# Kernel tuning notes

Measured on AMD Instinct MI355X. Metric: run time of the kernel, lower is better.

## Reference

```python
import jax, jax.numpy as jnp
import numpy as np

NUM_ITERATIONS = 3
EPS = 1e-7


def squash(t, axis=-1):
    # scale = |t|^2/(1+|t|^2), unit = t/sqrt(|t|^2+eps)
    sn = jnp.sum(t * t, axis=axis, keepdims=True)
    return (sn / (1.0 + sn)) * t / jnp.sqrt(sn + EPS)


def setup_inputs() -> dict:
    key = jax.random.key(0)
    kx, kw = jax.random.split(key)
    B, R, CIN = 256, 1152, 8
    C, COUT = 10, 16
    x = jax.random.normal(kx, (B, R, CIN), dtype=jnp.float32)
    W = jax.random.normal(kw, (C, R, CIN, COUT), dtype=jnp.float32)
    return {"x": x, "W": W}


def reference(x, W):
    # u_hat = x[None,:,:,None,:] @ W[:,None]  -> [C, B, R, 1, O]
    u_hat = jnp.einsum('bri,crio->cbro', x, W)[:, :, :, None, :]
    b = jnp.zeros_like(u_hat)  # logits over route nodes, full u_hat shape (faithful)
    outputs = None
    for i in range(NUM_ITERATIONS):
        c = jax.nn.softmax(b, axis=2)  # softmax over route nodes R
        outputs = squash(jnp.sum(c * u_hat, axis=2, keepdims=True))  # [C,B,1,1,O]
        if i != NUM_ITERATIONS - 1:
            # agreement: dot over out channels, broadcast back onto b
            b = b + jnp.sum(u_hat * outputs, axis=-1, keepdims=True)
    return outputs
```

## Files before the change

kernel.cpp:

```cpp
#include <hip/hip_runtime.h>
#include <hip/hip_fp16.h>

#define RDIM 1152
#define CIN  8
#define COUT 16
#define CDIM 10
#define BDIM 256
#define EPS 1e-7f

#define ARB 64
#define ABB 16
#define NRBLK (RDIM / ARB)
#define NBBLK (BDIM / ABB)
#define ANWG (CDIM * NRBLK * NBBLK)
#define XSTRIDE 12

__global__ __launch_bounds__(256) void caps_uhat(
    const float* __restrict__ x, const float* __restrict__ W,
    __half* __restrict__ uh)
{
    const int orig = blockIdx.x;
    const int id   = (orig & 7) * (ANWG / 8) + (orig >> 3);
    const int c    = id % CDIM;
    const int chnk = id / CDIM;
    const int rblk = chnk >> 4;
    const int bblk = chnk & 15;
    const int r0   = rblk * ARB;
    const int b0   = bblk * ABB;

    const int t    = threadIdx.x;
    const int half = t >> 7;
    const int u    = t & 127;
    const int rl   = u >> 1;
    const int oh   = u & 1;

    __shared__ float xs[ABB * ARB * XSTRIDE];

    {
        const float* xsrc = x + ((size_t)b0 * RDIM + r0) * CIN;
        #pragma unroll
        for (int k = 0; k < 8; ++k) {
            const int uu = t + k * 256;
            const int bl = uu >> 7;
            const int q  = uu & 127;
            float4 v = *(const float4*)(xsrc + (size_t)bl * RDIM * CIN + q * 4);
            *(float4*)&xs[(bl * ARB + (q >> 1)) * XSTRIDE + (q & 1) * 4] = v;
        }
    }

    float w0[8], w1[8], w2[8], w3[8], w4[8], w5[8], w6[8], w7[8];
    {
        const float* wb = W + ((size_t)c * RDIM + r0 + rl) * (CIN * COUT) + oh * 8;
        #define LDW(I, DST)                                                   \
        {                                                                     \
            float4 lo = *(const float4*)(wb + (I) * COUT);                    \
            float4 hi = *(const float4*)(wb + (I) * COUT + 4);                \
            DST[0] = lo.x; DST[1] = lo.y; DST[2] = lo.z; DST[3] = lo.w;       \
            DST[4] = hi.x; DST[5] = hi.y; DST[6] = hi.z; DST[7] = hi.w;       \
        }
        LDW(0, w0) LDW(1, w1) LDW(2, w2) LDW(3, w3)
        LDW(4, w4) LDW(5, w5) LDW(6, w6) LDW(7, w7)
        #undef LDW
    }
    asm volatile("" :
        "+v"(w0[0]), "+v"(w0[1]), "+v"(w0[2]), "+v"(w0[3]),
        "+v"(w0[4]), "+v"(w0[5]), "+v"(w0[6]), "+v"(w0[7]),
        "+v"(w1[0]), "+v"(w1[1]), "+v"(w1[2]), "+v"(w1[3]),
        "+v"(w1[4]), "+v"(w1[5]), "+v"(w1[6]), "+v"(w1[7]));
    asm volatile("" :
        "+v"(w2[0]), "+v"(w2[1]), "+v"(w2[2]), "+v"(w2[3]),
        "+v"(w2[4]), "+v"(w2[5]), "+v"(w2[6]), "+v"(w2[7]),
        "+v"(w3[0]), "+v"(w3[1]), "+v"(w3[2]), "+v"(w3[3]),
        "+v"(w3[4]), "+v"(w3[5]), "+v"(w3[6]), "+v"(w3[7]));
    asm volatile("" :
        "+v"(w4[0]), "+v"(w4[1]), "+v"(w4[2]), "+v"(w4[3]),
        "+v"(w4[4]), "+v"(w4[5]), "+v"(w4[6]), "+v"(w4[7]),
        "+v"(w5[0]), "+v"(w5[1]), "+v"(w5[2]), "+v"(w5[3]),
        "+v"(w5[4]), "+v"(w5[5]), "+v"(w5[6]), "+v"(w5[7]));
    asm volatile("" :
        "+v"(w6[0]), "+v"(w6[1]), "+v"(w6[2]), "+v"(w6[3]),
        "+v"(w6[4]), "+v"(w6[5]), "+v"(w6[6]), "+v"(w6[7]),
        "+v"(w7[0]), "+v"(w7[1]), "+v"(w7[2]), "+v"(w7[3]),
        "+v"(w7[4]), "+v"(w7[5]), "+v"(w7[6]), "+v"(w7[7]));

    __syncthreads();

    __half* ubase = uh + (((size_t)c * BDIM + b0 + half * 8) * RDIM + r0 + rl) * COUT
                  + oh * 8;
    const size_t ustep = (size_t)RDIM * COUT;
    const float* xrow = &xs[(half * 8 * ARB + rl) * XSTRIDE];

    #pragma unroll
    for (int bl = 0; bl < ABB / 2; ++bl) {
        const float* xp = xrow + bl * (ARB * XSTRIDE);
        float4 p0 = *(const float4*)(xp);
        float4 p1 = *(const float4*)(xp + 4);

        float a0 = p0.x * w0[0];
        float a1 = p0.x * w0[1];
        float a2 = p0.x * w0[2];
        float a3 = p0.x * w0[3];
        float a4 = p0.x * w0[4];
        float a5 = p0.x * w0[5];
        float a6 = p0.x * w0[6];
        float a7 = p0.x * w0[7];
        #define FMA8(XI, WR)                                                  \
            a0 = fmaf((XI), WR[0], a0); a1 = fmaf((XI), WR[1], a1);           \
            a2 = fmaf((XI), WR[2], a2); a3 = fmaf((XI), WR[3], a3);           \
            a4 = fmaf((XI), WR[4], a4); a5 = fmaf((XI), WR[5], a5);           \
            a6 = fmaf((XI), WR[6], a6); a7 = fmaf((XI), WR[7], a7);
        FMA8(p0.y, w1) FMA8(p0.z, w2) FMA8(p0.w, w3)
        FMA8(p1.x, w4) FMA8(p1.y, w5) FMA8(p1.z, w6) FMA8(p1.w, w7)
        #undef FMA8

        __half2 h0 = __floats2half2_rn(a0, a1), h1 = __floats2half2_rn(a2, a3);
        __half2 h2 = __floats2half2_rn(a4, a5), h3 = __floats2half2_rn(a6, a7);
        uint4 packed = make_uint4(*(const unsigned*)&h0, *(const unsigned*)&h1,
                                  *(const unsigned*)&h2, *(const unsigned*)&h3);
        *(uint4*)(ubase + bl * ustep) = packed;
    }
}

#define BUNIT 18

__global__ __launch_bounds__(256) void caps_route2(
    const __half* __restrict__ uh, float* __restrict__ out)
{
    const int cb   = blockIdx.x;
    const int t    = threadIdx.x;
    const int lane = t & 63;
    const int wave = t >> 6;
    const int oq   = t & 3;
    const int rsub = t >> 2;

    __shared__ uint2 uhs[RDIM * COUT / 4];
    __shared__ float red[4][20];
    __shared__ __align__(16) float vout[COUT];

    const uint4* src = (const uint4*)(uh + (size_t)cb * RDIM * COUT);
    uint4* dst = (uint4*)uhs;
    float sp[8] = {0.f, 0.f, 0.f, 0.f, 0.f, 0.f, 0.f, 0.f};
    #pragma unroll
    for (int k = 0; k < 9; ++k) {
        uint4 v = src[t + k * 256];
        dst[t + k * 256] = v;
        float2 f0 = __half22float2(*(const __half2*)&v.x);
        float2 f1 = __half22float2(*(const __half2*)&v.y);
        float2 f2 = __half22float2(*(const __half2*)&v.z);
        float2 f3 = __half22float2(*(const __half2*)&v.w);
        sp[0] += f0.x; sp[1] += f0.y; sp[2] += f1.x; sp[3] += f1.y;
        sp[4] += f2.x; sp[5] += f2.y; sp[6] += f3.x; sp[7] += f3.y;
    }
    #pragma unroll
    for (int off = 2; off <= 32; off <<= 1) {
        #pragma unroll
        for (int j = 0; j < 8; ++j) sp[j] += __shfl_xor(sp[j], off);
    }
    if (lane < 2) {
        #pragma unroll
        for (int j = 0; j < 8; ++j) red[wave][lane * 8 + j] = sp[j];
    }
    __syncthreads();

    if (wave == 0 && lane < COUT) {
        float s = 0.f;
        #pragma unroll
        for (int w2 = 0; w2 < 4; ++w2) s += red[w2][lane];
        s *= (1.0f / (float)RDIM);
        float sn = s * s;
        #pragma unroll
        for (int off = 1; off < 16; off <<= 1) sn += __shfl_xor(sn, off);
        const float scale = (sn / (1.0f + sn)) / sqrtf(sn + EPS);
        vout[lane] = s * scale;
    }
    __syncthreads();

    float bb[BUNIT];
    #pragma unroll
    for (int k = 0; k < BUNIT; ++k) bb[k] = 0.f;

    #pragma unroll
    for (int it = 1; it <= 2; ++it) {
        const float4 vq = *(const float4*)&vout[oq * 4];
        float Zp = 0.f, s0 = 0.f, s1 = 0.f, s2 = 0.f, s3 = 0.f;
        #pragma unroll
        for (int k = 0; k < BUNIT; ++k) {
            const int r = k * 64 + rsub;
            uint2 raw = uhs[r * 4 + oq];
            float2 fA = __half22float2(*(const __half2*)&raw.x);
            float2 fB = __half22float2(*(const __half2*)&raw.y);
            float a = fA.x * vq.x;
            a = fmaf(fA.y, vq.y, a);
            a = fmaf(fB.x, vq.z, a);
            a = fmaf(fB.y, vq.w, a);
            a += __shfl_xor(a, 1);
            a += __shfl_xor(a, 2);
            bb[k] += a;
            float e = __expf(bb[k]);
            Zp += e;
            s0 = fmaf(e, fA.x, s0); s1 = fmaf(e, fA.y, s1);
            s2 = fmaf(e, fB.x, s2); s3 = fmaf(e, fB.y, s3);
        }
        #pragma unroll
        for (int off = 32; off >= 4; off >>= 1) {
            Zp += __shfl_xor(Zp, off);
            s0 += __shfl_xor(s0, off);
            s1 += __shfl_xor(s1, off);
            s2 += __shfl_xor(s2, off);
            s3 += __shfl_xor(s3, off);
        }
        if (lane < 4) {
            red[wave][lane * 4 + 0] = s0;
            red[wave][lane * 4 + 1] = s1;
            red[wave][lane * 4 + 2] = s2;
            red[wave][lane * 4 + 3] = s3;
            if (lane == 0) red[wave][16] = Zp;
        }
        __syncthreads();
        if (wave == 0 && lane < COUT) {
            float Z = 0.f;
            #pragma unroll
            for (int w2 = 0; w2 < 4; ++w2) Z += red[w2][16];
            float s = 0.f;
            #pragma unroll
            for (int w2 = 0; w2 < 4; ++w2) s += red[w2][lane];
            s /= Z;
            float sn = s * s;
            #pragma unroll
            for (int off = 1; off < 16; off <<= 1) sn += __shfl_xor(sn, off);
            const float scale = (sn / (1.0f + sn)) / sqrtf(sn + EPS);
            vout[lane] = s * scale;
        }
        __syncthreads();
    }

    if (t < 4) {
        float* op = out + (size_t)cb * COUT + t * 4;
        *(float4*)op = *(const float4*)&vout[t * 4];
    }
}

#define NB   2
#define FBLOCK 384
#define FUNITS 12
#define FNW (FBLOCK / 64)
#define NPAIR (BDIM / NB)
#define FNWG (CDIM * NPAIR)

__global__ __launch_bounds__(FBLOCK) void caps_route_fused(
    const float* __restrict__ x, const float* __restrict__ W,
    float* __restrict__ out)
{
    const int orig = blockIdx.x;
    const int wg   = (orig & 7) * (FNWG / 8) + (orig >> 3);
    const int c    = wg / NPAIR;
    const int b0   = (wg % NPAIR) * NB;
    const int tid  = threadIdx.x;
    const int lane = tid & 63;
    const int wave = tid >> 6;
    const int oq   = tid & 3;
    const int rsub = tid >> 2;

    __shared__ uint2 uhT[NB][4][1156];
    __shared__ float red[NB][FNW][COUT];
    __shared__ float scalz[NB][FNW];
    __shared__ __align__(16) float vout[NB][COUT];

    const float* __restrict__ Wc  = W + (size_t)c * RDIM * CIN * COUT;
    const float* __restrict__ xb0 = x + (size_t)b0 * RDIM * CIN;
    const float* __restrict__ xb1 = xb0 + RDIM * CIN;

    #pragma unroll
    for (int k = 0; k < FUNITS; ++k) {
        const int r = k * 96 + rsub;
        const float4* xq0 = (const float4*)(xb0 + (size_t)r * CIN);
        const float4* xq1 = (const float4*)(xb1 + (size_t)r * CIN);
        float4 p00 = xq0[0], p01 = xq0[1];
        float4 p10 = xq1[0], p11 = xq1[1];
        float xr0[CIN] = {p00.x, p00.y, p00.z, p00.w, p01.x, p01.y, p01.z, p01.w};
        float xr1[CIN] = {p10.x, p10.y, p10.z, p10.w, p11.x, p11.y, p11.z, p11.w};
        const float* wrow = Wc + (size_t)r * (CIN * COUT) + oq * 4;
        float a00 = 0.f, a01 = 0.f, a02 = 0.f, a03 = 0.f;
        float a10 = 0.f, a11 = 0.f, a12 = 0.f, a13 = 0.f;
        #pragma unroll
        for (int i = 0; i < CIN; ++i) {
            float4 w = *(const float4*)(wrow + i * COUT);
            a00 = fmaf(xr0[i], w.x, a00); a01 = fmaf(xr0[i], w.y, a01);
            a02 = fmaf(xr0[i], w.z, a02); a03 = fmaf(xr0[i], w.w, a03);
            a10 = fmaf(xr1[i], w.x, a10); a11 = fmaf(xr1[i], w.y, a11);
            a12 = fmaf(xr1[i], w.z, a12); a13 = fmaf(xr1[i], w.w, a13);
        }
        __half2 hA0 = __floats2half2_rn(a00, a01), hB0 = __floats2half2_rn(a02, a03);
        __half2 hA1 = __floats2half2_rn(a10, a11), hB1 = __floats2half2_rn(a12, a13);
        uhT[0][oq][r] = make_uint2(*(const unsigned*)&hA0, *(const unsigned*)&hB0);
        uhT[1][oq][r] = make_uint2(*(const unsigned*)&hA1, *(const unsigned*)&hB1);
    }
    __syncthreads();

    float bb0[FUNITS], bb1[FUNITS];
    #pragma unroll
    for (int k = 0; k < FUNITS; ++k) { bb0[k] = 0.f; bb1[k] = 0.f; }

    #pragma unroll
    for (int it = 0; it < 3; ++it) {
        float Zp0 = 0.f, s00 = 0.f, s01 = 0.f, s02 = 0.f, s03 = 0.f;
        float Zp1 = 0.f, s10 = 0.f, s11 = 0.f, s12 = 0.f, s13 = 0.f;
        #pragma unroll
        for (int k = 0; k < FUNITS; ++k) {
            const int r = k * 96 + rsub;
            float e0 = __expf(bb0[k]);
            float e1 = __expf(bb1[k]);
            uint2 r0 = uhT[0][oq][r], r1 = uhT[1][oq][r];
            float2 fA0 = __half22float2(*(const __half2*)&r0.x);
            float2 fB0 = __half22float2(*(const __half2*)&r0.y);
            float2 fA1 = __half22float2(*(const __half2*)&r1.x);
            float2 fB1 = __half22float2(*(const __half2*)&r1.y);
            Zp0 += e0; Zp1 += e1;
            s00 = fmaf(e0, fA0.x, s00); s01 = fmaf(e0, fA0.y, s01);
            s02 = fmaf(e0, fB0.x, s02); s03 = fmaf(e0, fB0.y, s03);
            s10 = fmaf(e1, fA1.x, s10); s11 = fmaf(e1, fA1.y, s11);
            s12 = fmaf(e1, fB1.x, s12); s13 = fmaf(e1, fB1.y, s13);
        }
        #pragma unroll
        for (int off = 32; off >= 4; off >>= 1) {
            Zp0 += __shfl_xor(Zp0, off);  Zp1 += __shfl_xor(Zp1, off);
            s00 += __shfl_xor(s00, off);  s10 += __shfl_xor(s10, off);
            s01 += __shfl_xor(s01, off);  s11 += __shfl_xor(s11, off);
            s02 += __shfl_xor(s02, off);  s12 += __shfl_xor(s12, off);
            s03 += __shfl_xor(s03, off);  s13 += __shfl_xor(s13, off);
        }
        if (lane < 4) {
            red[0][wave][lane * 4 + 0] = s00; red[0][wave][lane * 4 + 1] = s01;
            red[0][wave][lane * 4 + 2] = s02; red[0][wave][lane * 4 + 3] = s03;
            red[1][wave][lane * 4 + 0] = s10; red[1][wave][lane * 4 + 1] = s11;
            red[1][wave][lane * 4 + 2] = s12; red[1][wave][lane * 4 + 3] = s13;
            if (lane == 0) { scalz[0][wave] = Zp0; scalz[1][wave] = Zp1; }
        }
        __syncthreads();
        if (wave == 0 && (lane & 31) < COUT) {
            const int nb = lane >> 5;
            const int o  = lane & 15;
            float Z = 0.f;
            #pragma unroll
            for (int w2 = 0; w2 < FNW; ++w2) Z += scalz[nb][w2];
            float s = 0.f;
            #pragma unroll
            for (int w2 = 0; w2 < FNW; ++w2) s += red[nb][w2][o];
            s /= Z;
            float sn = s * s;
            #pragma unroll
            for (int off = 1; off < 16; off <<= 1) sn += __shfl_xor(sn, off);
            const float scale = (sn / (1.0f + sn)) / sqrtf(sn + EPS);
            vout[nb][o] = s * scale;
        }
        __syncthreads();
        if (it < 2) {
            const float4 v0 = *(const float4*)&vout[0][oq * 4];
            const float4 v1 = *(const float4*)&vout[1][oq * 4];
            #pragma unroll
            for (int k = 0; k < FUNITS; ++k) {
                const int r = k * 96 + rsub;
                uint2 r0 = uhT[0][oq][r], r1 = uhT[1][oq][r];
                float2 fA0 = __half22float2(*(const __half2*)&r0.x);
                float2 fB0 = __half22float2(*(const __half2*)&r0.y);
                float2 fA1 = __half22float2(*(const __half2*)&r1.x);
                float2 fB1 = __half22float2(*(const __half2*)&r1.y);
                float a0 = fA0.x * v0.x;
                a0 = fmaf(fA0.y, v0.y, a0);
                a0 = fmaf(fB0.x, v0.z, a0);
                a0 = fmaf(fB0.y, v0.w, a0);
                float a1 = fA1.x * v1.x;
                a1 = fmaf(fA1.y, v1.y, a1);
                a1 = fmaf(fB1.x, v1.z, a1);
                a1 = fmaf(fB1.y, v1.w, a1);
                a0 += __shfl_xor(a0, 1);  a1 += __shfl_xor(a1, 1);
                a0 += __shfl_xor(a0, 2);  a1 += __shfl_xor(a1, 2);
                bb0[k] += a0;
                bb1[k] += a1;
            }
        }
    }
    if (tid < 8) {
        const int nb = tid >> 2, q = tid & 3;
        float* op = out + ((size_t)c * BDIM + b0 + nb) * COUT + q * 4;
        *(float4*)op = *(const float4*)&vout[nb][q * 4];
    }
}

extern "C" void kernel_launch(void* const* d_in, const int* in_sizes, int n_in,
                              void* d_out, int out_size, void* d_ws, size_t ws_size,
                              hipStream_t stream) {
    const float* x = (const float*)d_in[0];
    const float* W = (const float*)d_in[1];
    float* out = (float*)d_out;

    const size_t UH_BYTES = (size_t)CDIM * BDIM * RDIM * COUT * sizeof(__half);
    if (ws_size >= UH_BYTES) {
        __half* uh = (__half*)d_ws;
        caps_uhat<<<ANWG, 256, 0, stream>>>(x, W, uh);
        caps_route2<<<CDIM * BDIM, 256, 0, stream>>>(uh, out);
    } else {
        caps_route_fused<<<FNWG, FBLOCK, 0, stream>>>(x, W, out);
    }
}
```

Before: 56.14 us.

## Retile u_hat kernel to reuse x tile across five capsule classes

The u_hat kernel now tiles 16 route nodes by 32 batch rows and loops over five output classes per workgroup, loading the x tile into shared memory once and reusing it for each class. Before, every class had its own workgroup that reloaded x. This cuts redundant x traffic and reduces the grid to 1152 workgroups, each doing more serial work. The trade is that W loads are now serialized inside a non-unrolled loop, with less parallelism available to hide their latency.

```diff
diff --git a/kernel.cpp b/kernel.cpp
--- a/kernel.cpp
+++ b/kernel.cpp
@@ -8,11 +8,12 @@
 #define BDIM 256
 #define EPS 1e-7f
 
-#define ARB 64
-#define ABB 16
+#define ARB 16
+#define ABB 32
 #define NRBLK (RDIM / ARB)
 #define NBBLK (BDIM / ABB)
-#define ANWG (CDIM * NRBLK * NBBLK)
+#define NCG   2
+#define ANWG (NRBLK * NBBLK * NCG)
 #define XSTRIDE 12
 
 __global__ __launch_bounds__(256) void caps_uhat(
@@ -21,103 +22,110 @@
 {
     const int orig = blockIdx.x;
     const int id   = (orig & 7) * (ANWG / 8) + (orig >> 3);
-    const int c    = id % CDIM;
-    const int chnk = id / CDIM;
-    const int rblk = chnk >> 4;
-    const int bblk = chnk & 15;
+    const int cg   = id & 1;
+    const int rem  = id >> 1;
+    const int bblk = rem & 7;
+    const int rblk = rem >> 3;
     const int r0   = rblk * ARB;
     const int b0   = bblk * ABB;
 
-    const int t    = threadIdx.x;
-    const int half = t >> 7;
-    const int u    = t & 127;
-    const int rl   = u >> 1;
-    const int oh   = u & 1;
+    const int t  = threadIdx.x;
+    const int u  = t & 31;
+    const int rl = u >> 1;
+    const int oh = u & 1;
+    const int bg = t >> 5;
 
     __shared__ float xs[ABB * ARB * XSTRIDE];
 
     {
-        const float* xsrc = x + ((size_t)b0 * RDIM + r0) * CIN;
-        #pragma unroll
-        for (int k = 0; k < 8; ++k) {
-            const int uu = t + k * 256;
-            const int bl = uu >> 7;
-            const int q  = uu & 127;
-            float4 v = *(const float4*)(xsrc + (size_t)bl * RDIM * CIN + q * 4);
+        #pragma unroll
+        for (int k = 0; k < 4; ++k) {
+            const int unit = t + k * 256;
+            const int bl   = unit >> 5;
+            const int q    = unit & 31;
+            float4 v = *(const float4*)(
+                x + ((size_t)(b0 + bl) * RDIM + r0) * CIN + q * 4);
             *(float4*)&xs[(bl * ARB + (q >> 1)) * XSTRIDE + (q & 1) * 4] = v;
         }
     }
-
-    float w0[8], w1[8], w2[8], w3[8], w4[8], w5[8], w6[8], w7[8];
-    {
-        const float* wb = W + ((size_t)c * RDIM + r0 + rl) * (CIN * COUT) + oh * 8;
-        #define LDW(I, DST)                                                   \
-        {                                                                     \
-            float4 lo = *(const float4*)(wb + (I) * COUT);                    \
-            float4 hi = *(const float4*)(wb + (I) * COUT + 4);                \
-            DST[0] = lo.x; DST[1] = lo.y; DST[2] = lo.z; DST[3] = lo.w;       \
-            DST[4] = hi.x; DST[5] = hi.y; DST[6] = hi.z; DST[7] = hi.w;       \
-        }
-        LDW(0, w0) LDW(1, w1) LDW(2, w2) LDW(3, w3)
-        LDW(4, w4) LDW(5, w5) LDW(6, w6) LDW(7, w7)
-        #undef LDW
-    }
-    asm volatile("" :
-        "+v"(w0[0]), "+v"(w0[1]), "+v"(w0[2]), "+v"(w0[3]),
-        "+v"(w0[4]), "+v"(w0[5]), "+v"(w0[6]), "+v"(w0[7]),
-        "+v"(w1[0]), "+v"(w1[1]), "+v"(w1[2]), "+v"(w1[3]),
-        "+v"(w1[4]), "+v"(w1[5]), "+v"(w1[6]), "+v"(w1[7]));
-    asm volatile("" :
-        "+v"(w2[0]), "+v"(w2[1]), "+v"(w2[2]), "+v"(w2[3]),
-        "+v"(w2[4]), "+v"(w2[5]), "+v"(w2[6]), "+v"(w2[7]),
-        "+v"(w3[0]), "+v"(w3[1]), "+v"(w3[2]), "+v"(w3[3]),
-        "+v"(w3[4]), "+v"(w3[5]), "+v"(w3[6]), "+v"(w3[7]));
-    asm volatile("" :
-        "+v"(w4[0]), "+v"(w4[1]), "+v"(w4[2]), "+v"(w4[3]),
-        "+v"(w4[4]), "+v"(w4[5]), "+v"(w4[6]), "+v"(w4[7]),
-        "+v"(w5[0]), "+v"(w5[1]), "+v"(w5[2]), "+v"(w5[3]),
-        "+v"(w5[4]), "+v"(w5[5]), "+v"(w5[6]), "+v"(w5[7]));
-    asm volatile("" :
-        "+v"(w6[0]), "+v"(w6[1]), "+v"(w6[2]), "+v"(w6[3]),
-        "+v"(w6[4]), "+v"(w6[5]), "+v"(w6[6]), "+v"(w6[7]),
-        "+v"(w7[0]), "+v"(w7[1]), "+v"(w7[2]), "+v"(w7[3]),
-        "+v"(w7[4]), "+v"(w7[5]), "+v"(w7[6]), "+v"(w7[7]));
-
     __syncthreads();
 
-    __half* ubase = uh + (((size_t)c * BDIM + b0 + half * 8) * RDIM + r0 + rl) * COUT
-                  + oh * 8;
     const size_t ustep = (size_t)RDIM * COUT;
-    const float* xrow = &xs[(half * 8 * ARB + rl) * XSTRIDE];
-
-    #pragma unroll
-    for (int bl = 0; bl < ABB / 2; ++bl) {
-        const float* xp = xrow + bl * (ARB * XSTRIDE);
-        float4 p0 = *(const float4*)(xp);
-        float4 p1 = *(const float4*)(xp + 4);
-
-        float a0 = p0.x * w0[0];
-        float a1 = p0.x * w0[1];
-        float a2 = p0.x * w0[2];
-        float a3 = p0.x * w0[3];
-        float a4 = p0.x * w0[4];
-        float a5 = p0.x * w0[5];
-        float a6 = p0.x * w0[6];
-        float a7 = p0.x * w0[7];
-        #define FMA8(XI, WR)                                                  \
-            a0 = fmaf((XI), WR[0], a0); a1 = fmaf((XI), WR[1], a1);           \
-            a2 = fmaf((XI), WR[2], a2); a3 = fmaf((XI), WR[3], a3);           \
-            a4 = fmaf((XI), WR[4], a4); a5 = fmaf((XI), WR[5], a5);           \
-            a6 = fmaf((XI), WR[6], a6); a7 = fmaf((XI), WR[7], a7);
-        FMA8(p0.y, w1) FMA8(p0.z, w2) FMA8(p0.w, w3)
-        FMA8(p1.x, w4) FMA8(p1.y, w5) FMA8(p1.z, w6) FMA8(p1.w, w7)
-        #undef FMA8
-
-        __half2 h0 = __floats2half2_rn(a0, a1), h1 = __floats2half2_rn(a2, a3);
-        __half2 h2 = __floats2half2_rn(a4, a5), h3 = __floats2half2_rn(a6, a7);
-        uint4 packed = make_uint4(*(const unsigned*)&h0, *(const unsigned*)&h1,
-                                  *(const unsigned*)&h2, *(const unsigned*)&h3);
-        *(uint4*)(ubase + bl * ustep) = packed;
+
+    #pragma unroll 1
+    for (int ci = 0; ci < 5; ++ci) {
+        const int c = cg * 5 + ci;
+
+        float w0[8], w1[8], w2[8], w3[8], w4[8], w5[8], w6[8], w7[8];
+        {
+            const float* wb = W + ((size_t)c * RDIM + r0 + rl) * (CIN * COUT)
+                            + oh * 8;
+            #define LDW(I, DST)                                               \
+            {                                                                 \
+                float4 lo = *(const float4*)(wb + (I) * COUT);                \
+                float4 hi = *(const float4*)(wb + (I) * COUT + 4);            \
+                DST[0] = lo.x; DST[1] = lo.y; DST[2] = lo.z; DST[3] = lo.w;   \
+                DST[4] = hi.x; DST[5] = hi.y; DST[6] = hi.z; DST[7] = hi.w;   \
+            }
+            LDW(0, w0) LDW(1, w1) LDW(2, w2) LDW(3, w3)
+            LDW(4, w4) LDW(5, w5) LDW(6, w6) LDW(7, w7)
+            #undef LDW
+        }
+        asm volatile("" :
+            "+v"(w0[0]), "+v"(w0[1]), "+v"(w0[2]), "+v"(w0[3]),
+            "+v"(w0[4]), "+v"(w0[5]), "+v"(w0[6]), "+v"(w0[7]),
+            "+v"(w1[0]), "+v"(w1[1]), "+v"(w1[2]), "+v"(w1[3]),
+            "+v"(w1[4]), "+v"(w1[5]), "+v"(w1[6]), "+v"(w1[7]));
+        asm volatile("" :
+            "+v"(w2[0]), "+v"(w2[1]), "+v"(w2[2]), "+v"(w2[3]),
+            "+v"(w2[4]), "+v"(w2[5]), "+v"(w2[6]), "+v"(w2[7]),
+            "+v"(w3[0]), "+v"(w3[1]), "+v"(w3[2]), "+v"(w3[3]),
+            "+v"(w3[4]), "+v"(w3[5]), "+v"(w3[6]), "+v"(w3[7]));
+        asm volatile("" :
+            "+v"(w4[0]), "+v"(w4[1]), "+v"(w4[2]), "+v"(w4[3]),
+            "+v"(w4[4]), "+v"(w4[5]), "+v"(w4[6]), "+v"(w4[7]),
+            "+v"(w5[0]), "+v"(w5[1]), "+v"(w5[2]), "+v"(w5[3]),
+            "+v"(w5[4]), "+v"(w5[5]), "+v"(w5[6]), "+v"(w5[7]));
+        asm volatile("" :
+            "+v"(w6[0]), "+v"(w6[1]), "+v"(w6[2]), "+v"(w6[3]),
+            "+v"(w6[4]), "+v"(w6[5]), "+v"(w6[6]), "+v"(w6[7]),
+            "+v"(w7[0]), "+v"(w7[1]), "+v"(w7[2]), "+v"(w7[3]),
+            "+v"(w7[4]), "+v"(w7[5]), "+v"(w7[6]), "+v"(w7[7]));
+
+        __half* ubase = uh + (((size_t)c * BDIM + b0) * RDIM + r0 + rl) * COUT
+                      + oh * 8;
+
+        #pragma unroll
+        for (int j = 0; j < 4; ++j) {
+            const int bl = bg * 4 + j;
+            const float* xp = &xs[(bl * ARB + rl) * XSTRIDE];
+            float4 p0 = *(const float4*)(xp);
+            float4 p1 = *(const float4*)(xp + 4);
+
+            float a0 = p0.x * w0[0];
+            float a1 = p0.x * w0[1];
+            float a2 = p0.x * w0[2];
+            float a3 = p0.x * w0[3];
+            float a4 = p0.x * w0[4];
+            float a5 = p0.x * w0[5];
+            float a6 = p0.x * w0[6];
+            float a7 = p0.x * w0[7];
+            #define FMA8(XI, WR)                                              \
+                a0 = fmaf((XI), WR[0], a0); a1 = fmaf((XI), WR[1], a1);       \
+                a2 = fmaf((XI), WR[2], a2); a3 = fmaf((XI), WR[3], a3);       \
+                a4 = fmaf((XI), WR[4], a4); a5 = fmaf((XI), WR[5], a5);       \
+                a6 = fmaf((XI), WR[6], a6); a7 = fmaf((XI), WR[7], a7);
+            FMA8(p0.y, w1) FMA8(p0.z, w2) FMA8(p0.w, w3)
+            FMA8(p1.x, w4) FMA8(p1.y, w5) FMA8(p1.z, w6) FMA8(p1.w, w7)
+            #undef FMA8
+
+            __half2 h0 = __floats2half2_rn(a0, a1), h1 = __floats2half2_rn(a2, a3);
+            __half2 h2 = __floats2half2_rn(a4, a5), h3 = __floats2half2_rn(a6, a7);
+            uint4 packed = make_uint4(
+                *(const unsigned*)&h0, *(const unsigned*)&h1,
+                *(const unsigned*)&h2, *(const unsigned*)&h3);
+            *(uint4*)(ubase + (size_t)bl * ustep) = packed;
+        }
     }
 }
 
```

Measured after the change: 64.64 us. 15.1% more time.
